# Kernel optimization log

Measured on AMD Instinct MI355X. Metric: run time of the kernel, lower is better.

The kernel has to match this reference:

```python
import jax, jax.numpy as jnp
import numpy as np

H = 64        # hidden_dim
T = 3         # message passing steps
M = 3         # set2set steps
NEF = 4       # num_edge_features
NNF = 11      # num_node_features
NT = 12       # num_targets
N_NODES = 10000
N_EDGES = 50000
B = 256       # number of graphs


def setup_inputs() -> dict:
    key = jax.random.key(0)
    ks = jax.random.split(key, 32)

    def p(k, shape):
        fan_in = shape[-1]
        return jax.random.normal(k, shape, jnp.float32) / np.sqrt(fan_in)

    inp = {}
    inp['x'] = jax.random.normal(ks[0], (N_NODES, NNF), jnp.float32)
    inp['edge_attr'] = jax.random.uniform(ks[1], (N_EDGES, NEF), jnp.float32)
    inp['edge_index'] = jax.random.randint(ks[2], (2, N_EDGES), 0, N_NODES)
    inp['batch'] = jnp.sort(jax.random.randint(ks[3], (N_NODES,), 0, B))
    inp['batch_size'] = B
    # nn1: edge MLP -> per-edge HxH weight
    inp['w1a'] = p(ks[4], (H, NEF)); inp['b1a'] = jnp.zeros((H,), jnp.float32)
    inp['w1b'] = p(ks[5], (H, H));   inp['b1b'] = jnp.zeros((H,), jnp.float32)
    inp['w1c'] = p(ks[6], (H * H, H)); inp['b1c'] = jnp.zeros((H * H,), jnp.float32)
    # GRUCell
    inp['gru_wih'] = p(ks[7], (3 * H, H)); inp['gru_whh'] = p(ks[8], (3 * H, H))
    inp['gru_bih'] = jnp.zeros((3 * H,), jnp.float32); inp['gru_bhh'] = jnp.zeros((3 * H,), jnp.float32)
    # lin: (H + NNF) -> 2H
    inp['lin_w'] = p(ks[9], (2 * H, H + NNF)); inp['lin_b'] = jnp.zeros((2 * H,), jnp.float32)
    # Set2Set 2-layer LSTM: in_channels = 2H, input = 4H, hidden = 2H
    IC = 2 * H
    inp['lstm_wih0'] = p(ks[10], (4 * IC, 2 * IC)); inp['lstm_whh0'] = p(ks[11], (4 * IC, IC))
    inp['lstm_bih0'] = jnp.zeros((4 * IC,), jnp.float32); inp['lstm_bhh0'] = jnp.zeros((4 * IC,), jnp.float32)
    inp['lstm_wih1'] = p(ks[12], (4 * IC, IC)); inp['lstm_whh1'] = p(ks[13], (4 * IC, IC))
    inp['lstm_bih1'] = jnp.zeros((4 * IC,), jnp.float32); inp['lstm_bhh1'] = jnp.zeros((4 * IC,), jnp.float32)
    # nn2: 4H -> 8H -> num_targets
    inp['w2a'] = p(ks[14], (8 * H, 4 * H)); inp['b2a'] = jnp.zeros((8 * H,), jnp.float32)
    inp['w2b'] = p(ks[15], (NT, 8 * H)); inp['b2b'] = jnp.zeros((NT,), jnp.float32)
    return inp


def _gru(x, h, wih, whh, bih, bhh):
    gi = x @ wih.T + bih
    gh = h @ whh.T + bhh
    ir, iz, inn = jnp.split(gi, 3, axis=1)
    hr, hz, hn = jnp.split(gh, 3, axis=1)
    r = jax.nn.sigmoid(ir + hr)
    z = jax.nn.sigmoid(iz + hz)
    n = jnp.tanh(inn + r * hn)
    return (1.0 - z) * n + z * h


def _lstm(x, h, c, wih, whh, bih, bhh):
    g = x @ wih.T + bih + h @ whh.T + bhh
    i, f, gg, o = jnp.split(g, 4, axis=1)
    c_new = jax.nn.sigmoid(f) * c + jax.nn.sigmoid(i) * jnp.tanh(gg)
    h_new = jax.nn.sigmoid(o) * jnp.tanh(c_new)
    return h_new, c_new


def reference(x, edge_attr, w1a, b1a, w1b, b1b, w1c, b1c,
              gru_wih, gru_whh, gru_bih, gru_bhh, lin_w, lin_b,
              lstm_wih0, lstm_whh0, lstm_bih0, lstm_bhh0,
              lstm_wih1, lstm_whh1, lstm_bih1, lstm_bhh1,
              w2a, b2a, w2b, b2b, edge_index, batch, batch_size):
    N = x.shape[0]
    E = edge_attr.shape[0]
    src, dst = edge_index[0], edge_index[1]

    # pad node features into hidden state
    h = jnp.zeros((N, H), x.dtype).at[:, :x.shape[1]].set(x)

    # nn1 edge MLP -> per-edge (H, H) weight (edge_attr constant over T, hoisted)
    e1 = jax.nn.relu(edge_attr @ w1a.T + b1a)
    e1 = jax.nn.relu(e1 @ w1b.T + b1b)
    W_edge = (e1 @ w1c.T + b1c).reshape(E, H, H)  # [E, in, out]

    # T rounds of NNConv (gather -> per-edge matvec -> scatter-add) + GRU
    for _ in range(T):
        m_e = jnp.einsum('eh,eho->eo', h[src], W_edge)
        m = jax.ops.segment_sum(m_e, dst, num_segments=N)
        h = _gru(m, h, gru_wih, gru_whh, gru_bih, gru_bhh)

    h = jnp.concatenate([h, x], axis=1) @ lin_w.T + lin_b  # [N, 2H]

    # Set2Set readout with 2-layer LSTM
    IC = 2 * H
    q_star = jnp.zeros((batch_size, 2 * IC), h.dtype)
    h0 = jnp.zeros((batch_size, IC), h.dtype); c0 = jnp.zeros_like(h0)
    h1 = jnp.zeros_like(h0); c1 = jnp.zeros_like(h0)
    for _ in range(M):
        h0, c0 = _lstm(q_star, h0, c0, lstm_wih0, lstm_whh0, lstm_bih0, lstm_bhh0)
        h1, c1 = _lstm(h0, h1, c1, lstm_wih1, lstm_whh1, lstm_bih1, lstm_bhh1)
        q = h1  # [B, IC]
        e = jnp.sum(h * q[batch], axis=-1)  # [N]
        emax = jax.ops.segment_max(e, batch, num_segments=batch_size)
        a = jnp.exp(e - emax[batch])
        denom = jax.ops.segment_sum(a, batch, num_segments=batch_size)
        a = a / denom[batch]
        r = jax.ops.segment_sum(a[:, None] * h, batch, num_segments=batch_size)
        q_star = jnp.concatenate([q, r], axis=-1)  # [B, 4H]

    out = jax.nn.relu(q_star @ w2a.T + b2a) @ w2b.T + b2b
    return out
```

## Files before the change

kernel.cpp:

```cpp
#include <hip/hip_runtime.h>
#include <math.h>

#define NN 10000
#define NE 50000
#define BG 256
#define NNF 11
#define NT 12

typedef unsigned int u32;
typedef __attribute__((ext_vector_type(8))) short short8v;
typedef __attribute__((ext_vector_type(4))) float f32x4;

__device__ __forceinline__ float sigm(float x){ return 1.0f/(1.0f+__expf(-x)); }
__device__ __forceinline__ u32 f2bf(float f){
  u32 u = __float_as_uint(f);
  return (u + 0x7fffu + ((u>>16)&1u)) >> 16;
}
__device__ __forceinline__ float bf2f(u32 s){ return __uint_as_float(s<<16); }

__global__ __launch_bounds__(256) void k_h_init(const float* __restrict__ x, float* __restrict__ h,
                         unsigned short* __restrict__ hHi, unsigned short* __restrict__ hLo,
                         const float* __restrict__ b1c, float* __restrict__ hb,
                         float* __restrict__ m){
  __shared__ float sv[8][64];
  int t = threadIdx.x, w = t>>6, lane = t&63;
  int n0 = blockIdx.x*8 + w*2;
  #pragma unroll
  for (int q = 0; q < 2; ++q){
    int n = n0 + q;
    float v = (lane < NNF) ? x[n*NNF + lane] : 0.0f;
    h[n*64+lane] = v;
    u32 hv = f2bf(v);
    hHi[n*64+lane] = (unsigned short)hv;
    hLo[n*64+lane] = (unsigned short)f2bf(v - bf2f(hv));
    sv[2*w+q][lane] = v;
  }
  __syncthreads();
  #pragma unroll
  for (int q = 0; q < 2; ++q){
    int n = n0 + q;
    float acc = 0.f;
    #pragma unroll 8
    for (int i = 0; i < 64; ++i) acc = fmaf(sv[2*w+q][i], b1c[i*64+lane], acc);
    hb[n*64+lane] = acc;
    m[n*64+lane] = 0.f;
  }
}

__global__ void k_prep(const float* __restrict__ gwih, const float* __restrict__ gwhh,
                       const float* __restrict__ linw, const float* __restrict__ w1b,
                       const float* __restrict__ wih0, const float* __restrict__ whh0,
                       const float* __restrict__ wih1, const float* __restrict__ whh1,
                       const float* __restrict__ w2a,  const float* __restrict__ w1c,
                       float* __restrict__ wihT, float* __restrict__ whhT,
                       float* __restrict__ linT, unsigned short* __restrict__ w1bB,
                       float* __restrict__ wih0T, float* __restrict__ whh0T,
                       float* __restrict__ wih1T, float* __restrict__ whh1T,
                       float* __restrict__ w2aT, unsigned short* __restrict__ qtT,
                       int* __restrict__ deg, float* __restrict__ state0){
  int tid = blockIdx.x*256 + threadIdx.x;
  if (tid < 12288){ int i=tid>>6, j=tid&63; wihT[j*192+i]=gwih[tid]; return; }
  tid -= 12288;
  if (tid < 12288){ int i=tid>>6, j=tid&63; whhT[j*192+i]=gwhh[tid]; return; }
  tid -= 12288;
  if (tid < 9600){ int i=tid/75, j=tid-i*75; linT[j*128+i]=linw[tid]; return; }
  tid -= 9600;
  if (tid < 4096){ w1bB[tid] = (unsigned short)f2bf(w1b[tid]); return; }
  tid -= 4096;
  if (tid < 131072){ int i=tid>>8, j=tid&255; wih0T[j*512+i]=wih0[tid]; return; }
  tid -= 131072;
  if (tid < 65536){ int i=tid>>7, j=tid&127; whh0T[j*512+i]=whh0[tid]; return; }
  tid -= 65536;
  if (tid < 65536){ int i=tid>>7, j=tid&127; wih1T[j*512+i]=wih1[tid]; return; }
  tid -= 65536;
  if (tid < 65536){ int i=tid>>7, j=tid&127; whh1T[j*512+i]=whh1[tid]; return; }
  tid -= 65536;
  if (tid < 131072){ int i=tid>>8, j=tid&255; w2aT[j*512+i]=w2a[tid]; return; }
  tid -= 131072;
  if (tid < 262144){ int ko=tid>>6, hh=tid&63; int k=ko>>6, o=ko&63;
                     qtT[tid] = (unsigned short)f2bf(w1c[(hh*64+o)*64+k]); return; }
  tid -= 262144;
  if (tid < NN){ deg[tid] = 0; return; }
  tid -= NN;
  if (tid < 196608) state0[tid] = 0.f;
}

__global__ __launch_bounds__(256) void k_e1m(const float* __restrict__ ea,
                     const float* __restrict__ w1a, const float* __restrict__ b1a,
                     const unsigned short* __restrict__ w1bB, const float* __restrict__ b1b,
                     unsigned short* __restrict__ e1b){
  __shared__ unsigned short sHi[4][16][64], sLo[4][16][64];
  int t = threadIdx.x, w = t>>6, l = t&63;
  int c = l & 15, g = l >> 4;
  int eb = blockIdx.x*64 + w*16;
  float wa0=w1a[l*4+0], wa1=w1a[l*4+1], wa2=w1a[l*4+2], wa3=w1a[l*4+3];
  float bb1 = b1a[l];
  char* hbase = (char*)&sHi[w][0][0];
  char* lbase = (char*)&sLo[w][0][0];
  #pragma unroll
  for (int r = 0; r < 16; ++r){
    int e = eb + r; if (e >= NE) e = NE-1;
    float4 a = *(const float4*)&ea[e*4];
    float h1 = fmaxf(bb1 + a.x*wa0 + a.y*wa1 + a.z*wa2 + a.w*wa3, 0.f);
    u32 hv = f2bf(h1);
    u32 lv = f2bf(h1 - bf2f(hv));
    int wb = (r*128 + l*2) ^ ((r & 7) << 4);
    *(unsigned short*)(hbase + wb) = (unsigned short)hv;
    *(unsigned short*)(lbase + wb) = (unsigned short)lv;
  }
  __syncthreads();
  int xv = (c & 7) << 4;
  int rb0 = (c*128 + g*16) ^ xv;
  int rb1 = (c*128 + 64 + g*16) ^ xv;
  short8v aH0 = *(const short8v*)(hbase + rb0);
  short8v aH1 = *(const short8v*)(hbase + rb1);
  short8v aL0 = *(const short8v*)(lbase + rb0);
  short8v aL1 = *(const short8v*)(lbase + rb1);
  f32x4 acc[4];
  #pragma unroll
  for (int f = 0; f < 4; ++f){
    const short* wrow = (const short*)w1bB + (f*16 + c)*64 + g*8;
    short8v b0 = *(const short8v*)wrow;
    short8v b1 = *(const short8v*)(wrow + 32);
    acc[f] = f32x4{0.f,0.f,0.f,0.f};
    acc[f] = __builtin_amdgcn_mfma_f32_16x16x32_bf16(aH0, b0, acc[f], 0, 0, 0);
    acc[f] = __builtin_amdgcn_mfma_f32_16x16x32_bf16(aL0, b0, acc[f], 0, 0, 0);
    acc[f] = __builtin_amdgcn_mfma_f32_16x16x32_bf16(aH1, b1, acc[f], 0, 0, 0);
    acc[f] = __builtin_amdgcn_mfma_f32_16x16x32_bf16(aL1, b1, acc[f], 0, 0, 0);
  }
  #pragma unroll
  for (int f = 0; f < 4; ++f){
    float bb2 = b1b[f*16 + c];
    #pragma unroll
    for (int r = 0; r < 4; ++r){
      int e = eb + 4*g + r;
      if (e < NE)
        e1b[e*64 + f*16 + c] = (unsigned short)f2bf(fmaxf(acc[f][r] + bb2, 0.f));
    }
  }
}

__global__ __launch_bounds__(512) void k_P3(const unsigned short* __restrict__ hHi,
                      const unsigned short* __restrict__ hLo,
                      const unsigned short* __restrict__ qtT, u32* __restrict__ P2){
  __shared__ unsigned short sB[16384];
  int t = threadIdx.x; int w = t >> 6; int l = t & 63;
  int c = l & 15, g = l >> 4;
  int nt = blockIdx.x >> 4, kt = blockIdx.x & 15;
  int kob = kt*256;
  const char* qsrc = (const char*)qtT + (size_t)kob*128;
  char* sb = (char*)sB;
  #pragma unroll
  for (int r = 0; r < 4; ++r){
    int dstb = (r*512 + t)*16;
    int srcb = dstb ^ (((dstb >> 7) & 7) << 4);
    *(uint4*)(sb + dstb) = *(const uint4*)(qsrc + srcb);
  }
  int nb = nt*128 + w*16;
  int rowA = nb + c; if (rowA >= NN) rowA = NN-1;
  const short8v* aHiP = (const short8v*)((const short*)hHi + rowA*64 + g*8);
  const short8v* aLoP = (const short8v*)((const short*)hLo + rowA*64 + g*8);
  short8v aH0 = aHiP[0], aH1 = aHiP[4];
  short8v aL0 = aLoP[0], aL1 = aLoP[4];
  __syncthreads();
  int xv = (c & 7) << 4;
  f32x4 acc[16];
  #pragma unroll
  for (int f = 0; f < 16; ++f) acc[f] = f32x4{0.f,0.f,0.f,0.f};
  #pragma unroll
  for (int f = 0; f < 16; ++f){
    int baseb = f*2048 + c*128 + g*16;
    short8v b0 = *(const short8v*)(sb + (baseb ^ xv));
    short8v b1 = *(const short8v*)(sb + ((baseb + 64) ^ xv));
    acc[f] = __builtin_amdgcn_mfma_f32_16x16x32_bf16(aH0, b0, acc[f], 0, 0, 0);
    acc[f] = __builtin_amdgcn_mfma_f32_16x16x32_bf16(aL0, b0, acc[f], 0, 0, 0);
    acc[f] = __builtin_amdgcn_mfma_f32_16x16x32_bf16(aH1, b1, acc[f], 0, 0, 0);
    acc[f] = __builtin_amdgcn_mfma_f32_16x16x32_bf16(aL1, b1, acc[f], 0, 0, 0);
  }
  int k2b = kt*2;
  #pragma unroll
  for (int r = 0; r < 4; ++r){
    int node = nb + 4*g + r;
    if (node < NN){
      u32* dst = P2 + (size_t)node*2048;
      #pragma unroll
      for (int kk = 0; kk < 2; ++kk){
        uint4 v;
        v.x = f2bf(acc[8*kk+0][r]) | (f2bf(acc[8*kk+4][r]) << 16);
        v.y = f2bf(acc[8*kk+1][r]) | (f2bf(acc[8*kk+5][r]) << 16);
        v.z = f2bf(acc[8*kk+2][r]) | (f2bf(acc[8*kk+6][r]) << 16);
        v.w = f2bf(acc[8*kk+3][r]) | (f2bf(acc[8*kk+7][r]) << 16);
        *(uint4*)(dst + (k2b+kk)*64 + c*4) = v;
      }
    }
  }
}

__global__ void k_deg(const int* __restrict__ ei, int* __restrict__ deg){
  int e = blockIdx.x*256 + threadIdx.x;
  if (e >= NE) return;
  atomicAdd(&deg[ei[e]], 1);
}

__global__ __launch_bounds__(256) void k_scan(const int* __restrict__ deg, int* __restrict__ rowptr,
                       int* __restrict__ cursor){
  __shared__ int part[256];
  int t = threadIdx.x;
  int base = t*40;
  int s = 0;
  for (int i = 0; i < 40; ++i){ int idx = base+i; if (idx < NN) s += deg[idx]; }
  part[t] = s;
  __syncthreads();
  for (int off = 1; off < 256; off <<= 1){
    int v = (t >= off) ? part[t-off] : 0;
    __syncthreads();
    part[t] += v;
    __syncthreads();
  }
  int run = (t == 0) ? 0 : part[t-1];
  for (int i = 0; i < 40; ++i){
    int idx = base+i;
    if (idx < NN){ rowptr[idx] = run; cursor[idx] = run; run += deg[idx]; }
  }
  if (t == 255) rowptr[NN] = part[255];
}

__global__ void k_fill(const int* __restrict__ ei, int* __restrict__ cursor, int* __restrict__ csr_e){
  int e = blockIdx.x*256 + threadIdx.x;
  if (e >= NE) return;
  int s = ei[e];
  int pos = atomicAdd(&cursor[s], 1);
  csr_e[pos] = e;
}

__global__ __launch_bounds__(256, 2) void k_msg3(const int* __restrict__ rowptr,
                       const int* __restrict__ csr_e,
                       const int* __restrict__ ei, const u32* __restrict__ e1u,
                       const u32* __restrict__ P2, const float* __restrict__ hb,
                       float* __restrict__ m){
  int t = threadIdx.x; int w = t >> 6; int l = t & 63;
  int oo = ((l & 3) << 4) | (l >> 2);
  int n = blockIdx.x*4 + w;
  int jb = rowptr[n], je = rowptr[n+1];
  if (jb == je) return;
  float hbv = hb[n*64 + oo];
  const u32* Pn = P2 + (size_t)n*2048;
  u32 pr[32];
  #pragma unroll
  for (int k2 = 0; k2 < 32; ++k2) pr[k2] = Pn[k2*64 + l];
  int e = csr_e[jb];
  uint4 q[8];
  {
    const uint4* er4 = (const uint4*)(e1u + (size_t)e*32);
    #pragma unroll
    for (int i = 0; i < 8; ++i) q[i] = er4[i];
  }
  for (int j = jb; j < je; ++j){
    int dst = ei[NE + e];
    int en = (j+1 < je) ? csr_e[j+1] : e;
    uint4 qn[8];
    const uint4* ern = (const uint4*)(e1u + (size_t)en*32);
    #pragma unroll
    for (int i = 0; i < 8; ++i) qn[i] = ern[i];
    float a0 = hbv, a1 = 0.f, a2 = 0.f, a3 = 0.f;
    #pragma unroll
    for (int i = 0; i < 8; ++i){
      u32 w0 = q[i].x, w1 = q[i].y, w2 = q[i].z, w3 = q[i].w;
      u32 p0 = pr[4*i], p1 = pr[4*i+1], p2 = pr[4*i+2], p3 = pr[4*i+3];
      a0 = fmaf(bf2f(w0 & 0xffffu), bf2f(p0 & 0xffffu), a0);
      a0 = fmaf(bf2f(w0 >> 16),     bf2f(p0 >> 16),     a0);
      a1 = fmaf(bf2f(w1 & 0xffffu), bf2f(p1 & 0xffffu), a1);
      a1 = fmaf(bf2f(w1 >> 16),     bf2f(p1 >> 16),     a1);
      a2 = fmaf(bf2f(w2 & 0xffffu), bf2f(p2 & 0xffffu), a2);
      a2 = fmaf(bf2f(w2 >> 16),     bf2f(p2 >> 16),     a2);
      a3 = fmaf(bf2f(w3 & 0xffffu), bf2f(p3 & 0xffffu), a3);
      a3 = fmaf(bf2f(w3 >> 16),     bf2f(p3 >> 16),     a3);
    }
    atomicAdd(&m[dst*64 + oo], (a0+a1)+(a2+a3));
    #pragma unroll
    for (int i = 0; i < 8; ++i) q[i] = qn[i];
    e = en;
  }
}

__global__ __launch_bounds__(256) void k_gru(const float* __restrict__ m, float* __restrict__ h,
                     unsigned short* __restrict__ hHi, unsigned short* __restrict__ hLo,
                     const float* __restrict__ wihT, const float* __restrict__ whhT,
                     const float* __restrict__ bih, const float* __restrict__ bhh,
                     const float* __restrict__ b1c, float* __restrict__ hb,
                     float* __restrict__ mz){
  __shared__ float sm[8][64], sh[8][64], sv[8][64];
  int t = threadIdx.x, w = t>>6, lane = t&63;
  int n0 = blockIdx.x*8 + w*2;
  sm[2*w][lane]   = m[n0*64+lane];
  sm[2*w+1][lane] = m[(n0+1)*64+lane];
  sh[2*w][lane]   = h[n0*64+lane];
  sh[2*w+1][lane] = h[(n0+1)*64+lane];
  __syncthreads();
  float gi[2][3] = {{0,0,0},{0,0,0}}, gh[2][3] = {{0,0,0},{0,0,0}};
  #pragma unroll 2
  for (int i=0;i<64;++i){
    const float* wr = wihT + i*192;
    const float* ur = whhT + i*192;
    float w0=wr[lane], w1=wr[64+lane], w2=wr[128+lane];
    float u0=ur[lane], u1=ur[64+lane], u2=ur[128+lane];
    #pragma unroll
    for (int q=0;q<2;++q){
      float mi = sm[2*w+q][i], hi = sh[2*w+q][i];
      gi[q][0]=fmaf(mi,w0,gi[q][0]); gi[q][1]=fmaf(mi,w1,gi[q][1]); gi[q][2]=fmaf(mi,w2,gi[q][2]);
      gh[q][0]=fmaf(hi,u0,gh[q][0]); gh[q][1]=fmaf(hi,u1,gh[q][1]); gh[q][2]=fmaf(hi,u2,gh[q][2]);
    }
  }
  #pragma unroll
  for (int q=0;q<2;++q){
    int n = n0 + q;
    float r  = sigm(gi[q][0]+bih[lane]      + gh[q][0]+bhh[lane]);
    float z  = sigm(gi[q][1]+bih[64+lane]   + gh[q][1]+bhh[64+lane]);
    float nn_= tanhf(gi[q][2]+bih[128+lane] + r*(gh[q][2]+bhh[128+lane]));
    float ho = sh[2*w+q][lane];
    float hv = (1.f-z)*nn_ + z*ho;
    h[n*64+lane] = hv;
    u32 hv16 = f2bf(hv);
    hHi[n*64+lane] = (unsigned short)hv16;
    hLo[n*64+lane] = (unsigned short)f2bf(hv - bf2f(hv16));
    sv[2*w+q][lane] = hv;
  }
  __syncthreads();
  #pragma unroll
  for (int q=0;q<2;++q){
    int n = n0 + q;
    float acc = 0.f;
    #pragma unroll 8
    for (int i = 0; i < 64; ++i) acc = fmaf(sv[2*w+q][i], b1c[i*64+lane], acc);
    hb[n*64+lane] = acc;
    mz[n*64+lane] = 0.f;
  }
}

__global__ __launch_bounds__(256) void k_lin(const float* __restrict__ h, const float* __restrict__ x,
                     const float* __restrict__ linT, const float* __restrict__ lin_b, float* __restrict__ h2){
  __shared__ float sh[4][64];
  int t=threadIdx.x, w=t>>6, lane=t&63;
  int n = blockIdx.x*4 + w;
  sh[w][lane] = h[n*64+lane];
  __syncthreads();
  float a0 = lin_b[lane], a1 = lin_b[64+lane];
  #pragma unroll 4
  for (int i=0;i<64;++i){
    float v = sh[w][i];
    a0 = fmaf(v, linT[i*128+lane], a0);
    a1 = fmaf(v, linT[i*128+64+lane], a1);
  }
  #pragma unroll
  for (int i=0;i<11;++i){
    float v = x[n*NNF+i];
    a0 = fmaf(v, linT[(64+i)*128+lane], a0);
    a1 = fmaf(v, linT[(64+i)*128+64+lane], a1);
  }
  h2[n*128+lane] = a0;
  h2[n*128+64+lane] = a1;
}

__global__ void k_bounds(const int* __restrict__ batch, int* __restrict__ gstart){
  int b = blockIdx.x*256 + threadIdx.x;
  if (b > BG) return;
  int lo=0, hi=NN;
  while (lo < hi){ int mid=(lo+hi)>>1; if (batch[mid] < b) lo=mid+1; else hi=mid; }
  gstart[b]=lo;
}

__global__ __launch_bounds__(512) void k_lstm01(
    float* __restrict__ qstar,
    float* __restrict__ h0, float* __restrict__ c0,
    float* __restrict__ h1, float* __restrict__ c1,
    const float* __restrict__ wih0T, const float* __restrict__ whh0T,
    const float* __restrict__ bih0, const float* __restrict__ bhh0,
    const float* __restrict__ wih1T, const float* __restrict__ whh1T,
    const float* __restrict__ bih1, const float* __restrict__ bhh1){
  __shared__ float sin[256], s0[128], s1[128], sg[512];
  int b = blockIdx.x, j = threadIdx.x;
  if (j < 256) sin[j] = qstar[b*256 + j];
  else if (j < 384) s0[j-256] = h0[b*128 + (j-256)];
  else s1[j-384] = h1[b*128 + (j-384)];
  __syncthreads();
  {
    float a0 = bih0[j] + bhh0[j], a1 = 0.f, a2 = 0.f, a3 = 0.f;
    #pragma unroll
    for (int i = 0; i < 256; i += 4){
      a0 = fmaf(sin[i],   wih0T[(i)*512+j],   a0);
      a1 = fmaf(sin[i+1], wih0T[(i+1)*512+j], a1);
      a2 = fmaf(sin[i+2], wih0T[(i+2)*512+j], a2);
      a3 = fmaf(sin[i+3], wih0T[(i+3)*512+j], a3);
    }
    #pragma unroll
    for (int i = 0; i < 128; i += 4){
      a0 = fmaf(s0[i],   whh0T[(i)*512+j],   a0);
      a1 = fmaf(s0[i+1], whh0T[(i+1)*512+j], a1);
      a2 = fmaf(s0[i+2], whh0T[(i+2)*512+j], a2);
      a3 = fmaf(s0[i+3], whh0T[(i+3)*512+j], a3);
    }
    sg[j] = (a0+a1)+(a2+a3);
  }
  __syncthreads();
  if (j < 128){
    float ig = sigm(sg[j]), fg = sigm(sg[128+j]);
    float gg = tanhf(sg[256+j]), og = sigm(sg[384+j]);
    float c = fg*c0[b*128+j] + ig*gg;
    c0[b*128+j] = c;
    float hh = og*tanhf(c);
    h0[b*128+j] = hh;
    s0[j] = hh;
  }
  __syncthreads();
  {
    float a0 = bih1[j] + bhh1[j], a1 = 0.f, a2 = 0.f, a3 = 0.f;
    #pragma unroll
    for (int i = 0; i < 128; i += 4){
      a0 = fmaf(s0[i],   wih1T[(i)*512+j],   a0);
      a1 = fmaf(s0[i+1], wih1T[(i+1)*512+j], a1);
      a2 = fmaf(s0[i+2], wih1T[(i+2)*512+j], a2);
      a3 = fmaf(s0[i+3], wih1T[(i+3)*512+j], a3);
    }
    #pragma unroll
    for (int i = 0; i < 128; i += 4){
      a0 = fmaf(s1[i],   whh1T[(i)*512+j],   a0);
      a1 = fmaf(s1[i+1], whh1T[(i+1)*512+j], a1);
      a2 = fmaf(s1[i+2], whh1T[(i+2)*512+j], a2);
      a3 = fmaf(s1[i+3], whh1T[(i+3)*512+j], a3);
    }
    sg[j] = (a0+a1)+(a2+a3);
  }
  __syncthreads();
  if (j < 128){
    float ig = sigm(sg[j]), fg = sigm(sg[128+j]);
    float gg = tanhf(sg[256+j]), og = sigm(sg[384+j]);
    float c = fg*c1[b*128+j] + ig*gg;
    c1[b*128+j] = c;
    float hh = og*tanhf(c);
    h1[b*128+j] = hh;
    qstar[b*256+j] = hh;
  }
}

__global__ __launch_bounds__(256) void k_attn2(const float* __restrict__ h2,
                       const float* __restrict__ h1,
                       const int* __restrict__ gstart, float* __restrict__ qstar){
  __shared__ float pm[4], pl[4], pr[4][128];
  int b = blockIdx.x, t = threadIdx.x, w = t>>6, lane = t&63;
  float q0 = h1[b*128+lane], q1 = h1[b*128+64+lane];
  int s = gstart[b], e = gstart[b+1];
  float mrun = -3.0e38f, l = 0.f, r0 = 0.f, r1 = 0.f;
  for (int n = s + w; n < e; n += 4){
    float v0 = h2[n*128+lane], v1 = h2[n*128+64+lane];
    float d = fmaf(v0, q0, v1*q1);
    #pragma unroll
    for (int off = 32; off; off >>= 1) d += __shfl_xor(d, off);
    float mn = fmaxf(mrun, d);
    float sc = __expf(mrun - mn);
    float ww = __expf(d - mn);
    l = l*sc + ww;
    r0 = r0*sc + ww*v0;
    r1 = r1*sc + ww*v1;
    mrun = mn;
  }
  pr[w][lane] = r0; pr[w][64+lane] = r1;
  if (lane == 0){ pm[w] = mrun; pl[w] = l; }
  __syncthreads();
  if (t < 128){
    float M = fmaxf(fmaxf(pm[0],pm[1]), fmaxf(pm[2],pm[3]));
    float L = 0.f, R = 0.f;
    #pragma unroll
    for (int ww = 0; ww < 4; ++ww){
      float sc = __expf(pm[ww] - M);
      L = fmaf(pl[ww], sc, L);
      R = fmaf(pr[ww][t], sc, R);
    }
    float inv = (L > 0.f) ? 1.f/L : 0.f;
    qstar[b*256 + 128 + t] = R*inv;
  }
}

__global__ __launch_bounds__(512) void k_head(const float* __restrict__ qstar,
                      const float* __restrict__ w2aT, const float* __restrict__ b2a,
                      const float* __restrict__ w2b,  const float* __restrict__ b2b,
                      float* __restrict__ out){
  __shared__ float qs[256], sg[512];
  int b = blockIdx.x, j = threadIdx.x, w = j>>6, lane = j&63;
  if (j < 256) qs[j] = qstar[b*256 + j];
  __syncthreads();
  float a0 = b2a[j], a1 = 0.f, a2 = 0.f, a3 = 0.f;
  #pragma unroll
  for (int i = 0; i < 256; i += 4){
    a0 = fmaf(qs[i],   w2aT[(i)*512+j],   a0);
    a1 = fmaf(qs[i+1], w2aT[(i+1)*512+j], a1);
    a2 = fmaf(qs[i+2], w2aT[(i+2)*512+j], a2);
    a3 = fmaf(qs[i+3], w2aT[(i+3)*512+j], a3);
  }
  sg[j] = fmaxf((a0+a1)+(a2+a3), 0.f);
  __syncthreads();
  for (int jj = w; jj < NT; jj += 8){
    const float* wr = w2b + jj*512;
    float acc = 0.f;
    #pragma unroll
    for (int i = 0; i < 8; ++i) acc = fmaf(sg[lane+i*64], wr[lane+i*64], acc);
    #pragma unroll
    for (int off = 32; off; off >>= 1) acc += __shfl_xor(acc, off);
    if (lane == 0) out[b*NT+jj] = acc + b2b[jj];
  }
}

extern "C" void kernel_launch(void* const* d_in, const int* in_sizes, int n_in,
                              void* d_out, int out_size, void* d_ws, size_t ws_size,
                              hipStream_t stream) {
  const float* x    = (const float*)d_in[0];
  const float* ea   = (const float*)d_in[1];
  const int*   eidx = (const int*)d_in[2];
  const int*   batch= (const int*)d_in[3];
  const float* w1a  = (const float*)d_in[5];
  const float* b1a  = (const float*)d_in[6];
  const float* w1b  = (const float*)d_in[7];
  const float* b1b  = (const float*)d_in[8];
  const float* w1c  = (const float*)d_in[9];
  const float* b1c  = (const float*)d_in[10];
  const float* gwih = (const float*)d_in[11];
  const float* gwhh = (const float*)d_in[12];
  const float* gbih = (const float*)d_in[13];
  const float* gbhh = (const float*)d_in[14];
  const float* linw = (const float*)d_in[15];
  const float* linb = (const float*)d_in[16];
  const float* wih0 = (const float*)d_in[17];
  const float* whh0 = (const float*)d_in[18];
  const float* bih0 = (const float*)d_in[19];
  const float* bhh0 = (const float*)d_in[20];
  const float* wih1 = (const float*)d_in[21];
  const float* whh1 = (const float*)d_in[22];
  const float* bih1 = (const float*)d_in[23];
  const float* bhh1 = (const float*)d_in[24];
  const float* w2a  = (const float*)d_in[25];
  const float* b2a  = (const float*)d_in[26];
  const float* w2b  = (const float*)d_in[27];
  const float* b2b  = (const float*)d_in[28];
  float* out = (float*)d_out;

  char* p = (char*)d_ws;
  auto alloc = [&](size_t nbytes){ void* r = (void*)p; p += (nbytes + 255) & ~size_t(255); return r; };
  float* h    = (float*)alloc((size_t)NN*64*4);
  float* hb   = (float*)alloc((size_t)NN*64*4);
  float* m    = (float*)alloc((size_t)NN*64*4);
  float* h2   = (float*)alloc((size_t)NN*128*4);
  float* wihT = (float*)alloc(64*192*4);
  float* whhT = (float*)alloc(64*192*4);
  float* linT = (float*)alloc(75*128*4);
  unsigned short* w1bB = (unsigned short*)alloc(64*64*2);
  float* wih0T= (float*)alloc(256*512*4);
  float* whh0T= (float*)alloc(128*512*4);
  float* wih1T= (float*)alloc(128*512*4);
  float* whh1T= (float*)alloc(128*512*4);
  float* w2aT = (float*)alloc(256*512*4);
  float* qstar= (float*)alloc(256*256*4);
  float* h0   = (float*)alloc(256*128*4);
  float* c0   = (float*)alloc(256*128*4);
  float* h1s  = (float*)alloc(256*128*4);
  float* c1   = (float*)alloc(256*128*4);
  int*  gstart= (int*)alloc(257*4);
  unsigned short* e1b = (unsigned short*)alloc((size_t)NE*64*2);
  unsigned short* qtT = (unsigned short*)alloc((size_t)4096*64*2);
  unsigned short* hHi = (unsigned short*)alloc((size_t)NN*64*2);
  unsigned short* hLo = (unsigned short*)alloc((size_t)NN*64*2);
  int*  deg   = (int*)alloc((size_t)NN*4);
  int*  rowptr= (int*)alloc((size_t)(NN+1)*4);
  int*  cursor= (int*)alloc((size_t)NN*4);
  int*  csr_e = (int*)alloc((size_t)NE*4);
  u32*  P2    = (u32*)alloc((size_t)NN*2048*4);

  k_prep<<<3773, 256, 0, stream>>>(gwih, gwhh, linw, w1b, wih0, whh0, wih1, whh1,
                                   w2a, w1c, wihT, whhT, linT, w1bB, wih0T, whh0T,
                                   wih1T, whh1T, w2aT, qtT, deg, qstar);
  k_h_init<<<1250, 256, 0, stream>>>(x, h, hHi, hLo, b1c, hb, m);
  k_e1m<<<782, 256, 0, stream>>>(ea, w1a, b1a, w1bB, b1b, e1b);
  k_bounds<<<2, 256, 0, stream>>>(batch, gstart);
  k_deg<<<196, 256, 0, stream>>>(eidx, deg);
  k_scan<<<1, 256, 0, stream>>>(deg, rowptr, cursor);
  k_fill<<<196, 256, 0, stream>>>(eidx, cursor, csr_e);

  for (int t = 0; t < 3; ++t) {
    k_P3<<<79*16, 512, 0, stream>>>(hHi, hLo, qtT, P2);
    k_msg3<<<2500, 256, 0, stream>>>(rowptr, csr_e, eidx, (const u32*)e1b, P2, hb, m);
    k_gru<<<1250, 256, 0, stream>>>(m, h, hHi, hLo, wihT, whhT, gbih, gbhh, b1c, hb, m);
  }

  k_lin<<<2500, 256, 0, stream>>>(h, x, linT, linb, h2);

  for (int s = 0; s < 3; ++s) {
    k_lstm01<<<256, 512, 0, stream>>>(qstar, h0, c0, h1s, c1,
                                      wih0T, whh0T, bih0, bhh0,
                                      wih1T, whh1T, bih1, bhh1);
    k_attn2<<<256, 256, 0, stream>>>(h2, h1s, gstart, qstar);
  }

  k_head<<<256, 512, 0, stream>>>(qstar, w2aT, b2a, w2b, b2b, out);
}
```

Before: 508.0 us.

## Batch Set2Set LSTM over 16 graphs using bf16 split-precision MFMA

Replaces the per-graph FP32 LSTM kernel with one where each block processes 16 graphs and computes gates via bf16 MFMA. Activations are split into hi/lo bf16 parts to retain near-FP32 precision, and weights are pre-converted to bf16 in their original row-major layout. This cuts the repeated weight reads from 256 blocks to 16 and uses matrix cores. The trade-off is a grid of only 16 blocks and bf16 rounding of the weights.

```diff
diff --git a/kernel.cpp b/kernel.cpp
--- a/kernel.cpp
+++ b/kernel.cpp
@@ -17,6 +17,18 @@
   return (u + 0x7fffu + ((u>>16)&1u)) >> 16;
 }
 __device__ __forceinline__ float bf2f(u32 s){ return __uint_as_float(s<<16); }
+
+__device__ __forceinline__ void packHiLo8(const float* p, short8v& hi, short8v& lo){
+  float4 v0 = *(const float4*)p;
+  float4 v1 = *(const float4*)(p+4);
+  float vv[8] = {v0.x,v0.y,v0.z,v0.w,v1.x,v1.y,v1.z,v1.w};
+  #pragma unroll
+  for (int i=0;i<8;++i){
+    u32 hv = f2bf(vv[i]);
+    ((unsigned short*)&hi)[i] = (unsigned short)hv;
+    ((unsigned short*)&lo)[i] = (unsigned short)f2bf(vv[i]-bf2f(hv));
+  }
+}
 
 __global__ __launch_bounds__(256) void k_h_init(const float* __restrict__ x, float* __restrict__ h,
                          unsigned short* __restrict__ hHi, unsigned short* __restrict__ hLo,
@@ -54,8 +66,8 @@
                        const float* __restrict__ w2a,  const float* __restrict__ w1c,
                        float* __restrict__ wihT, float* __restrict__ whhT,
                        float* __restrict__ linT, unsigned short* __restrict__ w1bB,
-                       float* __restrict__ wih0T, float* __restrict__ whh0T,
-                       float* __restrict__ wih1T, float* __restrict__ whh1T,
+                       unsigned short* __restrict__ wih0B, unsigned short* __restrict__ whh0B,
+                       unsigned short* __restrict__ wih1B, unsigned short* __restrict__ whh1B,
                        float* __restrict__ w2aT, unsigned short* __restrict__ qtT,
                        int* __restrict__ deg, float* __restrict__ state0){
   int tid = blockIdx.x*256 + threadIdx.x;
@@ -67,13 +79,13 @@
   tid -= 9600;
   if (tid < 4096){ w1bB[tid] = (unsigned short)f2bf(w1b[tid]); return; }
   tid -= 4096;
-  if (tid < 131072){ int i=tid>>8, j=tid&255; wih0T[j*512+i]=wih0[tid]; return; }
+  if (tid < 131072){ wih0B[tid] = (unsigned short)f2bf(wih0[tid]); return; }
   tid -= 131072;
-  if (tid < 65536){ int i=tid>>7, j=tid&127; whh0T[j*512+i]=whh0[tid]; return; }
+  if (tid < 65536){ whh0B[tid] = (unsigned short)f2bf(whh0[tid]); return; }
   tid -= 65536;
-  if (tid < 65536){ int i=tid>>7, j=tid&127; wih1T[j*512+i]=wih1[tid]; return; }
+  if (tid < 65536){ wih1B[tid] = (unsigned short)f2bf(wih1[tid]); return; }
   tid -= 65536;
-  if (tid < 65536){ int i=tid>>7, j=tid&127; whh1T[j*512+i]=whh1[tid]; return; }
+  if (tid < 65536){ whh1B[tid] = (unsigned short)f2bf(whh1[tid]); return; }
   tid -= 65536;
   if (tid < 131072){ int i=tid>>8, j=tid&255; w2aT[j*512+i]=w2a[tid]; return; }
   tid -= 131072;
@@ -369,76 +381,110 @@
   gstart[b]=lo;
 }
 
-__global__ __launch_bounds__(512) void k_lstm01(
+__global__ __launch_bounds__(512) void k_lstmM(
     float* __restrict__ qstar,
     float* __restrict__ h0, float* __restrict__ c0,
     float* __restrict__ h1, float* __restrict__ c1,
-    const float* __restrict__ wih0T, const float* __restrict__ whh0T,
+    const unsigned short* __restrict__ wih0B, const unsigned short* __restrict__ whh0B,
     const float* __restrict__ bih0, const float* __restrict__ bhh0,
-    const float* __restrict__ wih1T, const float* __restrict__ whh1T,
+    const unsigned short* __restrict__ wih1B, const unsigned short* __restrict__ whh1B,
     const float* __restrict__ bih1, const float* __restrict__ bhh1){
-  __shared__ float sin[256], s0[128], s1[128], sg[512];
-  int b = blockIdx.x, j = threadIdx.x;
-  if (j < 256) sin[j] = qstar[b*256 + j];
-  else if (j < 384) s0[j-256] = h0[b*128 + (j-256)];
-  else s1[j-384] = h1[b*128 + (j-384)];
-  __syncthreads();
+  __shared__ float sOld0[16][132], sOld1[16][132], sNew0[16][132];
+  int t = threadIdx.x, w = t>>6, l = t&63;
+  int c = l & 15, gq = l >> 4;
+  int gb = blockIdx.x*16;
+  int jj = w*16 + c;
   {
-    float a0 = bih0[j] + bhh0[j], a1 = 0.f, a2 = 0.f, a3 = 0.f;
-    #pragma unroll
-    for (int i = 0; i < 256; i += 4){
-      a0 = fmaf(sin[i],   wih0T[(i)*512+j],   a0);
-      a1 = fmaf(sin[i+1], wih0T[(i+1)*512+j], a1);
-      a2 = fmaf(sin[i+2], wih0T[(i+2)*512+j], a2);
-      a3 = fmaf(sin[i+3], wih0T[(i+3)*512+j], a3);
-    }
-    #pragma unroll
-    for (int i = 0; i < 128; i += 4){
-      a0 = fmaf(s0[i],   whh0T[(i)*512+j],   a0);
-      a1 = fmaf(s0[i+1], whh0T[(i+1)*512+j], a1);
-      a2 = fmaf(s0[i+2], whh0T[(i+2)*512+j], a2);
-      a3 = fmaf(s0[i+3], whh0T[(i+3)*512+j], a3);
-    }
-    sg[j] = (a0+a1)+(a2+a3);
-  }
-  __syncthreads();
-  if (j < 128){
-    float ig = sigm(sg[j]), fg = sigm(sg[128+j]);
-    float gg = tanhf(sg[256+j]), og = sigm(sg[384+j]);
-    float c = fg*c0[b*128+j] + ig*gg;
-    c0[b*128+j] = c;
-    float hh = og*tanhf(c);
-    h0[b*128+j] = hh;
-    s0[j] = hh;
-  }
-  __syncthreads();
+    int row = t >> 5, col4 = (t & 31)*4;
+    float4 v0 = *(const float4*)&h0[(gb+row)*128 + col4];
+    float4 v1 = *(const float4*)&h1[(gb+row)*128 + col4];
+    *(float4*)&sOld0[row][col4] = v0;
+    *(float4*)&sOld1[row][col4] = v1;
+  }
+  short8v qH[8], qL[8];
   {
-    float a0 = bih1[j] + bhh1[j], a1 = 0.f, a2 = 0.f, a3 = 0.f;
-    #pragma unroll
-    for (int i = 0; i < 128; i += 4){
-      a0 = fmaf(s0[i],   wih1T[(i)*512+j],   a0);
-      a1 = fmaf(s0[i+1], wih1T[(i+1)*512+j], a1);
-      a2 = fmaf(s0[i+2], wih1T[(i+2)*512+j], a2);
-      a3 = fmaf(s0[i+3], wih1T[(i+3)*512+j], a3);
-    }
-    #pragma unroll
-    for (int i = 0; i < 128; i += 4){
-      a0 = fmaf(s1[i],   whh1T[(i)*512+j],   a0);
-      a1 = fmaf(s1[i+1], whh1T[(i+1)*512+j], a1);
-      a2 = fmaf(s1[i+2], whh1T[(i+2)*512+j], a2);
-      a3 = fmaf(s1[i+3], whh1T[(i+3)*512+j], a3);
-    }
-    sg[j] = (a0+a1)+(a2+a3);
-  }
-  __syncthreads();
-  if (j < 128){
-    float ig = sigm(sg[j]), fg = sigm(sg[128+j]);
-    float gg = tanhf(sg[256+j]), og = sigm(sg[384+j]);
-    float c = fg*c1[b*128+j] + ig*gg;
-    c1[b*128+j] = c;
-    float hh = og*tanhf(c);
-    h1[b*128+j] = hh;
-    qstar[b*256+j] = hh;
+    const float* qrow = qstar + (size_t)(gb + c)*256;
+    #pragma unroll
+    for (int kk = 0; kk < 8; ++kk)
+      packHiLo8(qrow + kk*32 + gq*8, qH[kk], qL[kk]);
+  }
+  __syncthreads();
+  short8v hH[4], hL[4];
+  #pragma unroll
+  for (int kk = 0; kk < 4; ++kk)
+    packHiLo8(&sOld0[c][kk*32 + gq*8], hH[kk], hL[kk]);
+  f32x4 acc[4];
+  #pragma unroll
+  for (int qd = 0; qd < 4; ++qd){
+    int j = qd*128 + jj;
+    f32x4 a = f32x4{0.f,0.f,0.f,0.f};
+    const short* wr = (const short*)wih0B + (size_t)j*256 + gq*8;
+    #pragma unroll
+    for (int kk = 0; kk < 8; ++kk){
+      short8v b = *(const short8v*)(wr + kk*32);
+      a = __builtin_amdgcn_mfma_f32_16x16x32_bf16(qH[kk], b, a, 0, 0, 0);
+      a = __builtin_amdgcn_mfma_f32_16x16x32_bf16(qL[kk], b, a, 0, 0, 0);
+    }
+    const short* ur = (const short*)whh0B + (size_t)j*128 + gq*8;
+    #pragma unroll
+    for (int kk = 0; kk < 4; ++kk){
+      short8v b = *(const short8v*)(ur + kk*32);
+      a = __builtin_amdgcn_mfma_f32_16x16x32_bf16(hH[kk], b, a, 0, 0, 0);
+      a = __builtin_amdgcn_mfma_f32_16x16x32_bf16(hL[kk], b, a, 0, 0, 0);
+    }
+    float bb = bih0[j] + bhh0[j];
+    a[0]+=bb; a[1]+=bb; a[2]+=bb; a[3]+=bb;
+    acc[qd] = a;
+  }
+  #pragma unroll
+  for (int r = 0; r < 4; ++r){
+    int b = gb + 4*gq + r;
+    float cc = c0[b*128 + jj];
+    float ig = sigm(acc[0][r]), fg = sigm(acc[1][r]);
+    float gg = tanhf(acc[2][r]), og = sigm(acc[3][r]);
+    float cn = fg*cc + ig*gg;
+    c0[b*128 + jj] = cn;
+    float hn = og*tanhf(cn);
+    h0[b*128 + jj] = hn;
+    sNew0[4*gq + r][jj] = hn;
+  }
+  __syncthreads();
+  short8v g0H[4], g0L[4], g1H[4], g1L[4];
+  #pragma unroll
+  for (int kk = 0; kk < 4; ++kk){
+    packHiLo8(&sNew0[c][kk*32 + gq*8], g0H[kk], g0L[kk]);
+    packHiLo8(&sOld1[c][kk*32 + gq*8], g1H[kk], g1L[kk]);
+  }
+  #pragma unroll
+  for (int qd = 0; qd < 4; ++qd){
+    int j = qd*128 + jj;
+    f32x4 a = f32x4{0.f,0.f,0.f,0.f};
+    const short* wr = (const short*)wih1B + (size_t)j*128 + gq*8;
+    const short* ur = (const short*)whh1B + (size_t)j*128 + gq*8;
+    #pragma unroll
+    for (int kk = 0; kk < 4; ++kk){
+      short8v b0 = *(const short8v*)(wr + kk*32);
+      a = __builtin_amdgcn_mfma_f32_16x16x32_bf16(g0H[kk], b0, a, 0, 0, 0);
+      a = __builtin_amdgcn_mfma_f32_16x16x32_bf16(g0L[kk], b0, a, 0, 0, 0);
+      short8v b1 = *(const short8v*)(ur + kk*32);
+      a = __builtin_amdgcn_mfma_f32_16x16x32_bf16(g1H[kk], b1, a, 0, 0, 0);
+      a = __builtin_amdgcn_mfma_f32_16x16x32_bf16(g1L[kk], b1, a, 0, 0, 0);
+    }
+    float bb = bih1[j] + bhh1[j];
+    a[0]+=bb; a[1]+=bb; a[2]+=bb; a[3]+=bb;
+    acc[qd] = a;
+  }
+  #pragma unroll
+  for (int r = 0; r < 4; ++r){
+    int b = gb + 4*gq + r;
+    float cc = c1[b*128 + jj];
+    float ig = sigm(acc[0][r]), fg = sigm(acc[1][r]);
+    float gg = tanhf(acc[2][r]), og = sigm(acc[3][r]);
+    float cn = fg*cc + ig*gg;
+    c1[b*128 + jj] = cn;
+    float hn = og*tanhf(cn);
+    h1[b*128 + jj] = hn;
+    qstar[b*256 + jj] = hn;
   }
 }
 
@@ -552,10 +598,10 @@
   float* whhT = (float*)alloc(64*192*4);
   float* linT = (float*)alloc(75*128*4);
   unsigned short* w1bB = (unsigned short*)alloc(64*64*2);
-  float* wih0T= (float*)alloc(256*512*4);
-  float* whh0T= (float*)alloc(128*512*4);
-  float* wih1T= (float*)alloc(128*512*4);
-  float* whh1T= (float*)alloc(128*512*4);
+  unsigned short* wih0B= (unsigned short*)alloc(131072*2);
+  unsigned short* whh0B= (unsigned short*)alloc(65536*2);
+  unsigned short* wih1B= (unsigned short*)alloc(65536*2);
+  unsigned short* whh1B= (unsigned short*)alloc(65536*2);
   float* w2aT = (float*)alloc(256*512*4);
   float* qstar= (float*)alloc(256*256*4);
   float* h0   = (float*)alloc(256*128*4);
@@ -574,8 +620,8 @@
   u32*  P2    = (u32*)alloc((size_t)NN*2048*4);
 
   k_prep<<<3773, 256, 0, stream>>>(gwih, gwhh, linw, w1b, wih0, whh0, wih1, whh1,
-                                   w2a, w1c, wihT, whhT, linT, w1bB, wih0T, whh0T,
-                                   wih1T, whh1T, w2aT, qtT, deg, qstar);
+                                   w2a, w1c, wihT, whhT, linT, w1bB, wih0B, whh0B,
+                                   wih1B, whh1B, w2aT, qtT, deg, qstar);
   k_h_init<<<1250, 256, 0, stream>>>(x, h, hHi, hLo, b1c, hb, m);
   k_e1m<<<782, 256, 0, stream>>>(ea, w1a, b1a, w1bB, b1b, e1b);
   k_bounds<<<2, 256, 0, stream>>>(batch, gstart);
@@ -592,9 +638,9 @@
   k_lin<<<2500, 256, 0, stream>>>(h, x, linT, linb, h2);
 
   for (int s = 0; s < 3; ++s) {
-    k_lstm01<<<256, 512, 0, stream>>>(qstar, h0, c0, h1s, c1,
-                                      wih0T, whh0T, bih0, bhh0,
-                                      wih1T, whh1T, bih1, bhh1);
+    k_lstmM<<<16, 512, 0, stream>>>(qstar, h0, c0, h1s, c1,
+                                    wih0B, whh0B, bih0, bhh0,
+                                    wih1B, whh1B, bih1, bhh1);
     k_attn2<<<256, 256, 0, stream>>>(h2, h1s, gstart, qstar);
   }
 
```

Result: slower. 532.6 us (+4.8%).

## Batch four graphs per LSTM block with gate-interleaved float4 weights

Applied to the files above, without the earlier changes.

The LSTM weights are repacked so the four gates (i,f,g,o) for each hidden unit sit together as a float4. Each thread then computes all four gates of one unit and applies the cell update in registers, without the shared-memory gate exchange. Each 512-thread block now handles four graphs, so every weight load is reused across four batch rows, but the grid shrinks from 256 to 64 blocks. This cuts weight traffic and barriers in exchange for less parallelism across the GPU.

```diff
diff --git a/kernel.cpp b/kernel.cpp
--- a/kernel.cpp
+++ b/kernel.cpp
@@ -54,8 +54,8 @@
                        const float* __restrict__ w2a,  const float* __restrict__ w1c,
                        float* __restrict__ wihT, float* __restrict__ whhT,
                        float* __restrict__ linT, unsigned short* __restrict__ w1bB,
-                       float* __restrict__ wih0T, float* __restrict__ whh0T,
-                       float* __restrict__ wih1T, float* __restrict__ whh1T,
+                       float* __restrict__ p0i, float* __restrict__ p0h,
+                       float* __restrict__ p1i, float* __restrict__ p1h,
                        float* __restrict__ w2aT, unsigned short* __restrict__ qtT,
                        int* __restrict__ deg, float* __restrict__ state0){
   int tid = blockIdx.x*256 + threadIdx.x;
@@ -67,14 +67,26 @@
   tid -= 9600;
   if (tid < 4096){ w1bB[tid] = (unsigned short)f2bf(w1b[tid]); return; }
   tid -= 4096;
-  if (tid < 131072){ int i=tid>>8, j=tid&255; wih0T[j*512+i]=wih0[tid]; return; }
-  tid -= 131072;
-  if (tid < 65536){ int i=tid>>7, j=tid&127; whh0T[j*512+i]=whh0[tid]; return; }
-  tid -= 65536;
-  if (tid < 65536){ int i=tid>>7, j=tid&127; wih1T[j*512+i]=wih1[tid]; return; }
-  tid -= 65536;
-  if (tid < 65536){ int i=tid>>7, j=tid&127; whh1T[j*512+i]=whh1[tid]; return; }
-  tid -= 65536;
+  if (tid < 32768){ int i=tid>>7, j=tid&127;
+    float4 v = make_float4(wih0[(j)*256+i], wih0[(128+j)*256+i],
+                           wih0[(256+j)*256+i], wih0[(384+j)*256+i]);
+    *(float4*)&p0i[tid*4] = v; return; }
+  tid -= 32768;
+  if (tid < 16384){ int i=tid>>7, j=tid&127;
+    float4 v = make_float4(whh0[(j)*128+i], whh0[(128+j)*128+i],
+                           whh0[(256+j)*128+i], whh0[(384+j)*128+i]);
+    *(float4*)&p0h[tid*4] = v; return; }
+  tid -= 16384;
+  if (tid < 16384){ int i=tid>>7, j=tid&127;
+    float4 v = make_float4(wih1[(j)*128+i], wih1[(128+j)*128+i],
+                           wih1[(256+j)*128+i], wih1[(384+j)*128+i]);
+    *(float4*)&p1i[tid*4] = v; return; }
+  tid -= 16384;
+  if (tid < 16384){ int i=tid>>7, j=tid&127;
+    float4 v = make_float4(whh1[(j)*128+i], whh1[(128+j)*128+i],
+                           whh1[(256+j)*128+i], whh1[(384+j)*128+i]);
+    *(float4*)&p1h[tid*4] = v; return; }
+  tid -= 16384;
   if (tid < 131072){ int i=tid>>8, j=tid&255; w2aT[j*512+i]=w2a[tid]; return; }
   tid -= 131072;
   if (tid < 262144){ int ko=tid>>6, hh=tid&63; int k=ko>>6, o=ko&63;
@@ -369,76 +381,77 @@
   gstart[b]=lo;
 }
 
-__global__ __launch_bounds__(512) void k_lstm01(
+__global__ __launch_bounds__(512) void k_lstm4(
     float* __restrict__ qstar,
     float* __restrict__ h0, float* __restrict__ c0,
     float* __restrict__ h1, float* __restrict__ c1,
-    const float* __restrict__ wih0T, const float* __restrict__ whh0T,
+    const f32x4* __restrict__ p0i, const f32x4* __restrict__ p0h,
+    const f32x4* __restrict__ p1i, const f32x4* __restrict__ p1h,
     const float* __restrict__ bih0, const float* __restrict__ bhh0,
-    const float* __restrict__ wih1T, const float* __restrict__ whh1T,
     const float* __restrict__ bih1, const float* __restrict__ bhh1){
-  __shared__ float sin[256], s0[128], s1[128], sg[512];
-  int b = blockIdx.x, j = threadIdx.x;
-  if (j < 256) sin[j] = qstar[b*256 + j];
-  else if (j < 384) s0[j-256] = h0[b*128 + (j-256)];
-  else s1[j-384] = h1[b*128 + (j-384)];
-  __syncthreads();
+  __shared__ float sq[4][256], s0[4][128], s1[4][128], sn[4][128];
+  int t = threadIdx.x, g = t>>7, j = t&127;
+  int b = blockIdx.x*4 + g;
+  sq[t>>8][t&255]            = qstar[blockIdx.x*1024 + t];
+  sq[(t+512)>>8][(t+512)&255]= qstar[blockIdx.x*1024 + 512 + t];
+  s0[g][j] = h0[b*128+j];
+  s1[g][j] = h1[b*128+j];
+  __syncthreads();
+  f32x4 A0 = f32x4{bih0[j]+bhh0[j], bih0[128+j]+bhh0[128+j],
+                   bih0[256+j]+bhh0[256+j], bih0[384+j]+bhh0[384+j]};
+  f32x4 A1 = f32x4{0,0,0,0}, A2 = f32x4{0,0,0,0}, A3 = f32x4{0,0,0,0};
+  const float* q = sq[g];
+  #pragma unroll 8
+  for (int i = 0; i < 256; i += 4){
+    A0 += q[i]   * p0i[(i)*128+j];
+    A1 += q[i+1] * p0i[(i+1)*128+j];
+    A2 += q[i+2] * p0i[(i+2)*128+j];
+    A3 += q[i+3] * p0i[(i+3)*128+j];
+  }
+  const float* hp = s0[g];
+  #pragma unroll 8
+  for (int i = 0; i < 128; i += 4){
+    A0 += hp[i]   * p0h[(i)*128+j];
+    A1 += hp[i+1] * p0h[(i+1)*128+j];
+    A2 += hp[i+2] * p0h[(i+2)*128+j];
+    A3 += hp[i+3] * p0h[(i+3)*128+j];
+  }
+  f32x4 A = (A0+A1)+(A2+A3);
   {
-    float a0 = bih0[j] + bhh0[j], a1 = 0.f, a2 = 0.f, a3 = 0.f;
-    #pragma unroll
-    for (int i = 0; i < 256; i += 4){
-      a0 = fmaf(sin[i],   wih0T[(i)*512+j],   a0);
-      a1 = fmaf(sin[i+1], wih0T[(i+1)*512+j], a1);
-      a2 = fmaf(sin[i+2], wih0T[(i+2)*512+j], a2);
-      a3 = fmaf(sin[i+3], wih0T[(i+3)*512+j], a3);
-    }
-    #pragma unroll
-    for (int i = 0; i < 128; i += 4){
-      a0 = fmaf(s0[i],   whh0T[(i)*512+j],   a0);
-      a1 = fmaf(s0[i+1], whh0T[(i+1)*512+j], a1);
-      a2 = fmaf(s0[i+2], whh0T[(i+2)*512+j], a2);
-      a3 = fmaf(s0[i+3], whh0T[(i+3)*512+j], a3);
-    }
-    sg[j] = (a0+a1)+(a2+a3);
-  }
-  __syncthreads();
-  if (j < 128){
-    float ig = sigm(sg[j]), fg = sigm(sg[128+j]);
-    float gg = tanhf(sg[256+j]), og = sigm(sg[384+j]);
-    float c = fg*c0[b*128+j] + ig*gg;
-    c0[b*128+j] = c;
-    float hh = og*tanhf(c);
-    h0[b*128+j] = hh;
-    s0[j] = hh;
-  }
-  __syncthreads();
+    float cc = c0[b*128+j];
+    float ig = sigm(A[0]), fg = sigm(A[1]), gg = tanhf(A[2]), og = sigm(A[3]);
+    float cn = fg*cc + ig*gg;
+    c0[b*128+j] = cn;
+    float hn = og*tanhf(cn);
+    h0[b*128+j] = hn;
+    sn[g][j] = hn;
+  }
+  __syncthreads();
+  f32x4 B0 = f32x4{bih1[j]+bhh1[j], bih1[128+j]+bhh1[128+j],
+                   bih1[256+j]+bhh1[256+j], bih1[384+j]+bhh1[384+j]};
+  f32x4 B1 = f32x4{0,0,0,0}, B2 = f32x4{0,0,0,0}, B3 = f32x4{0,0,0,0};
+  const float* np = sn[g];
+  const float* op = s1[g];
+  #pragma unroll 8
+  for (int i = 0; i < 128; i += 4){
+    B0 += np[i]   * p1i[(i)*128+j];
+    B1 += np[i+1] * p1i[(i+1)*128+j];
+    B2 += np[i+2] * p1i[(i+2)*128+j];
+    B3 += np[i+3] * p1i[(i+3)*128+j];
+    B0 += op[i]   * p1h[(i)*128+j];
+    B1 += op[i+1] * p1h[(i+1)*128+j];
+    B2 += op[i+2] * p1h[(i+2)*128+j];
+    B3 += op[i+3] * p1h[(i+3)*128+j];
+  }
+  f32x4 B = (B0+B1)+(B2+B3);
   {
-    float a0 = bih1[j] + bhh1[j], a1 = 0.f, a2 = 0.f, a3 = 0.f;
-    #pragma unroll
-    for (int i = 0; i < 128; i += 4){
-      a0 = fmaf(s0[i],   wih1T[(i)*512+j],   a0);
-      a1 = fmaf(s0[i+1], wih1T[(i+1)*512+j], a1);
-      a2 = fmaf(s0[i+2], wih1T[(i+2)*512+j], a2);
-      a3 = fmaf(s0[i+3], wih1T[(i+3)*512+j], a3);
-    }
-    #pragma unroll
-    for (int i = 0; i < 128; i += 4){
-      a0 = fmaf(s1[i],   whh1T[(i)*512+j],   a0);
-      a1 = fmaf(s1[i+1], whh1T[(i+1)*512+j], a1);
-      a2 = fmaf(s1[i+2], whh1T[(i+2)*512+j], a2);
-      a3 = fmaf(s1[i+3], whh1T[(i+3)*512+j], a3);
-    }
-    sg[j] = (a0+a1)+(a2+a3);
-  }
-  __syncthreads();
-  if (j < 128){
-    float ig = sigm(sg[j]), fg = sigm(sg[128+j]);
-    float gg = tanhf(sg[256+j]), og = sigm(sg[384+j]);
-    float c = fg*c1[b*128+j] + ig*gg;
-    c1[b*128+j] = c;
-    float hh = og*tanhf(c);
-    h1[b*128+j] = hh;
-    qstar[b*256+j] = hh;
+    float cc = c1[b*128+j];
+    float ig = sigm(B[0]), fg = sigm(B[1]), gg = tanhf(B[2]), og = sigm(B[3]);
+    float cn = fg*cc + ig*gg;
+    c1[b*128+j] = cn;
+    float hn = og*tanhf(cn);
+    h1[b*128+j] = hn;
+    qstar[b*256+j] = hn;
   }
 }
 
@@ -552,10 +565,10 @@
   float* whhT = (float*)alloc(64*192*4);
   float* linT = (float*)alloc(75*128*4);
   unsigned short* w1bB = (unsigned short*)alloc(64*64*2);
-  float* wih0T= (float*)alloc(256*512*4);
-  float* whh0T= (float*)alloc(128*512*4);
-  float* wih1T= (float*)alloc(128*512*4);
-  float* whh1T= (float*)alloc(128*512*4);
+  float* p0i  = (float*)alloc(131072*4);
+  float* p0h  = (float*)alloc(65536*4);
+  float* p1i  = (float*)alloc(65536*4);
+  float* p1h  = (float*)alloc(65536*4);
   float* w2aT = (float*)alloc(256*512*4);
   float* qstar= (float*)alloc(256*256*4);
   float* h0   = (float*)alloc(256*128*4);
@@ -573,9 +586,9 @@
   int*  csr_e = (int*)alloc((size_t)NE*4);
   u32*  P2    = (u32*)alloc((size_t)NN*2048*4);
 
-  k_prep<<<3773, 256, 0, stream>>>(gwih, gwhh, linw, w1b, wih0, whh0, wih1, whh1,
-                                   w2a, w1c, wihT, whhT, linT, w1bB, wih0T, whh0T,
-                                   wih1T, whh1T, w2aT, qtT, deg, qstar);
+  k_prep<<<2813, 256, 0, stream>>>(gwih, gwhh, linw, w1b, wih0, whh0, wih1, whh1,
+                                   w2a, w1c, wihT, whhT, linT, w1bB, p0i, p0h,
+                                   p1i, p1h, w2aT, qtT, deg, qstar);
   k_h_init<<<1250, 256, 0, stream>>>(x, h, hHi, hLo, b1c, hb, m);
   k_e1m<<<782, 256, 0, stream>>>(ea, w1a, b1a, w1bB, b1b, e1b);
   k_bounds<<<2, 256, 0, stream>>>(batch, gstart);
@@ -592,9 +605,10 @@
   k_lin<<<2500, 256, 0, stream>>>(h, x, linT, linb, h2);
 
   for (int s = 0; s < 3; ++s) {
-    k_lstm01<<<256, 512, 0, stream>>>(qstar, h0, c0, h1s, c1,
-                                      wih0T, whh0T, bih0, bhh0,
-                                      wih1T, whh1T, bih1, bhh1);
+    k_lstm4<<<64, 512, 0, stream>>>(qstar, h0, c0, h1s, c1,
+                                    (const f32x4*)p0i, (const f32x4*)p0h,
+                                    (const f32x4*)p1i, (const f32x4*)p1h,
+                                    bih0, bhh0, bih1, bhh1);
     k_attn2<<<256, 256, 0, stream>>>(h2, h1s, gstart, qstar);
   }
 
```

Measured after the change: 598.3 us. 17.8% more time.
